# Kernel tuning notes

Measured on AMD Instinct MI355X. Metric: run time of the kernel, lower is better.

## Reference

```python
import jax, jax.numpy as jnp
import numpy as np

N_NODES = 50000
N_EDGES = 25000  # hyperedges
NNZ = 400000     # incidence pairs


def _segment_mean(x, idx, num_segments):
    s = jax.ops.segment_sum(x, idx, num_segments=num_segments)
    cnt = jax.ops.segment_sum(jnp.ones((x.shape[0], 1), x.dtype), idx, num_segments=num_segments)
    return s / jnp.maximum(cnt, 1.0)


def _unigcn_conv(X, W, vertex, edges, degE, degV):
    # X: [N, Cin] -> [N, Cout]
    X = X @ W                                   # linear (no bias)
    Xve = X[vertex]                             # gather per incidence [nnz, C]
    Xe = _segment_mean(Xve, edges, N_EDGES)     # first_aggregate='mean' over hyperedges
    Xe = Xe * degE                              # [M,1] scale
    Xev = Xe[edges]                             # gather back [nnz, C]
    Xv = jax.ops.segment_sum(Xev, vertex, num_segments=N_NODES)
    return Xv * degV                            # [N,1] scale


def setup_inputs() -> dict:
    key = jax.random.key(0)
    ks = jax.random.split(key, 8)
    nfeat, nhid_total, nclass = 512, 512, 40
    def glorot(k, fan_in, fan_out):
        std = np.sqrt(6.0 / (fan_in + fan_out))
        return jax.random.uniform(k, (fan_in, fan_out), jnp.float32, -std, std)
    return {
        "X": jax.random.normal(ks[0], (N_NODES, nfeat), jnp.float32),
        "vertex": jax.random.randint(ks[1], (NNZ,), 0, N_NODES, jnp.int32),
        "edges": jax.random.randint(ks[2], (NNZ,), 0, N_EDGES, jnp.int32),
        "W1": glorot(ks[3], nfeat, nhid_total),
        "W2": glorot(ks[4], nhid_total, nhid_total),
        "Wout": glorot(ks[5], nhid_total, nclass),
        "degE": jax.random.uniform(ks[6], (N_EDGES, 1), jnp.float32, 0.1, 1.0),
        "degV": jax.random.uniform(ks[7], (N_NODES, 1), jnp.float32, 0.1, 1.0),
    }


def reference(X, vertex, edges, W1, W2, Wout, degE, degV):
    # dropout layers are identity at eval (rates = 0)
    X = jax.nn.relu(_unigcn_conv(X, W1, vertex, edges, degE, degV))
    X = jax.nn.relu(_unigcn_conv(X, W2, vertex, edges, degE, degV))
    X = _unigcn_conv(X, Wout, vertex, edges, degE, degV)
    return jax.nn.log_softmax(X, axis=1)
```

## Files before the change

kernel.cpp:

```cpp
#include <hip/hip_runtime.h>

#define N_NODES 50000
#define N_EDGES_C 25000
#define NNZ_C 400000
#define SCHUNK 2048

typedef __bf16 bf16;
typedef __bf16 bf16x8 __attribute__((ext_vector_type(8)));
typedef __bf16 bf16x4 __attribute__((ext_vector_type(4)));
typedef float f32x4 __attribute__((ext_vector_type(4)));

typedef __attribute__((address_space(1))) const void as1_cvoid;
typedef __attribute__((address_space(3))) void as3_void;

__device__ __forceinline__ void gload_lds16(const bf16* g, bf16* l) {
  __builtin_amdgcn_global_load_lds((as1_cvoid*)g, (as3_void*)l, 16, 0, 0);
}

__global__ void hist_kernel(const int* __restrict__ vtx, const int* __restrict__ edg,
                            int* __restrict__ cntV, int* __restrict__ cntE, int nnz) {
  int i = blockIdx.x * blockDim.x + threadIdx.x;
  if (i < nnz) {
    atomicAdd(&cntV[vtx[i]], 1);
    atomicAdd(&cntE[edg[i]], 1);
  }
}

__global__ void scan_part2(const int* __restrict__ cntE, const int* __restrict__ cntV,
                           int* __restrict__ partE, int* __restrict__ partV,
                           int nbE) {
  __shared__ int red[256];
  const int t = threadIdx.x;
  const int isV = (blockIdx.x >= nbE);
  const int b = isV ? (blockIdx.x - nbE) : blockIdx.x;
  const int* cnt = isV ? cntV : cntE;
  const int n = isV ? N_NODES : N_EDGES_C;
  const int base = b * SCHUNK + t * 8;
  int s = 0;
#pragma unroll
  for (int q = 0; q < 8; ++q) {
    int i = base + q;
    if (i < n) s += cnt[i];
  }
  red[t] = s;
  __syncthreads();
  for (int d = 128; d > 0; d >>= 1) {
    if (t < d) red[t] += red[t + d];
    __syncthreads();
  }
  if (t == 0) (isV ? partV : partE)[b] = red[0];
}

__global__ void scan_mid2(int* __restrict__ partE, int* __restrict__ partV,
                          int* __restrict__ eoff, int* __restrict__ voff,
                          int nbE, int nbV) {
  const int wv = threadIdx.x >> 6;
  const int lane = threadIdx.x & 63;
  int* part = wv ? partV : partE;
  int* off = wv ? voff : eoff;
  const int np = wv ? nbV : nbE;
  const int n = wv ? N_NODES : N_EDGES_C;
  int orig = (lane < np) ? part[lane] : 0;
  int v = orig;
  for (int o = 1; o < 64; o <<= 1) {
    int x = __shfl_up(v, o);
    if (lane >= o) v += x;
  }
  if (lane < np) part[lane] = v - orig;
  if (lane == 63) off[n] = v;
}

__global__ void scan_final2(const int* __restrict__ cntE, const int* __restrict__ cntV,
                            const int* __restrict__ partE, const int* __restrict__ partV,
                            int* __restrict__ eoff, int* __restrict__ voff, int nbE) {
  __shared__ int tsum[256];
  const int t = threadIdx.x;
  const int isV = (blockIdx.x >= nbE);
  const int b = isV ? (blockIdx.x - nbE) : blockIdx.x;
  const int* cnt = isV ? cntV : cntE;
  const int* part = isV ? partV : partE;
  int* off = isV ? voff : eoff;
  const int n = isV ? N_NODES : N_EDGES_C;
  const int base = b * SCHUNK + t * 8;
  int loc[8];
  int s = 0;
#pragma unroll
  for (int q = 0; q < 8; ++q) {
    int i = base + q;
    loc[q] = (i < n) ? cnt[i] : 0;
    s += loc[q];
  }
  tsum[t] = s;
  __syncthreads();
  for (int d = 1; d < 256; d <<= 1) {
    int x = (t >= d) ? tsum[t - d] : 0;
    __syncthreads();
    tsum[t] += x;
    __syncthreads();
  }
  int run = part[b] + ((t > 0) ? tsum[t - 1] : 0);
#pragma unroll
  for (int q = 0; q < 8; ++q) {
    int i = base + q;
    if (i < n) off[i] = run;
    run += loc[q];
  }
}

__global__ void scatter_kernel(const int* __restrict__ vtx, const int* __restrict__ edg,
                               const int* __restrict__ eoff, const int* __restrict__ voff,
                               int* __restrict__ curE, int* __restrict__ curV,
                               int* __restrict__ evtx, int* __restrict__ vedg, int nnz) {
  int i = blockIdx.x * blockDim.x + threadIdx.x;
  if (i < nnz) {
    int e = edg[i], v = vtx[i];
    int p = atomicAdd(&curE[e], 1);
    evtx[eoff[e] + p] = v;
    int q = atomicAdd(&curV[v], 1);
    vedg[voff[v] + q] = e;
  }
}

__global__ void prep_conv(const float* __restrict__ W1, const float* __restrict__ W2,
                          const float* __restrict__ Wout, const float* __restrict__ X,
                          bf16* __restrict__ Wt1, bf16* __restrict__ Wt2,
                          bf16* __restrict__ Wt3, bf16* __restrict__ Xb) {
  const int b = blockIdx.x;
  const int t = threadIdx.x;
  if (b < 1024) {
    int idx = b * 256 + t;
    int n = idx >> 9, k = idx & 511;
    Wt1[idx] = (bf16)W1[(size_t)k * 512 + n];
  } else if (b < 2048) {
    int idx = (b - 1024) * 256 + t;
    int n = idx >> 9, k = idx & 511;
    Wt2[idx] = (bf16)W2[(size_t)k * 512 + n];
  } else if (b < 2304) {
    int idx = (b - 2048) * 256 + t;
    int n = idx >> 9, k = idx & 511;
    Wt3[idx] = (n < 40) ? (bf16)Wout[(size_t)k * 40 + n] : (bf16)0.0f;
  } else {
    size_t i = ((size_t)(b - 2304) * 256 + t) * 8;
    float4 v0 = *(const float4*)(X + i);
    float4 v1 = *(const float4*)(X + i + 4);
    bf16x8 o;
    o[0] = (bf16)v0.x; o[1] = (bf16)v0.y; o[2] = (bf16)v0.z; o[3] = (bf16)v0.w;
    o[4] = (bf16)v1.x; o[5] = (bf16)v1.y; o[6] = (bf16)v1.z; o[7] = (bf16)v1.w;
    *(bf16x8*)(Xb + i) = o;
  }
}

template <int BF16OUT>
__global__ __launch_bounds__(256) void gemm_bf16_kernel(
    const bf16* __restrict__ A, const bf16* __restrict__ B,
    float* __restrict__ Cf, bf16* __restrict__ Cb, int M, int K, int ldC, int Nstore) {
  __shared__ bf16 Al[2][128][64];
  __shared__ bf16 Bl[2][128][64];
  const int t = threadIdx.x;
  const int n0 = blockIdx.x * 128;
  const int m0 = blockIdx.y * 128;
  const int w = t >> 6, lane = t & 63;
  const int wr = w >> 1, wc = w & 1;
  const int lr = lane & 15;
  const int ls = lane >> 4;

  f32x4 acc[4][4];
#pragma unroll
  for (int m = 0; m < 4; ++m)
#pragma unroll
    for (int n = 0; n < 4; ++n) acc[m][n] = (f32x4){0.f, 0.f, 0.f, 0.f};

  const int srow8 = lane >> 3;
  const int scol = ((lane & 7) ^ srow8) << 3;

  const bf16* Abase = A + (size_t)m0 * K;
  const bf16* Bbase = B + (size_t)n0 * K;

#define STAGE(tile, bsel)                                                        \
  {                                                                              \
    const int kk_ = (tile) * 64;                                                 \
    _Pragma("unroll")                                                            \
    for (int q = 0; q < 4; ++q) {                                                \
      const int row = w * 32 + q * 8 + srow8;                                    \
      gload_lds16(Abase + (size_t)row * K + kk_ + scol, &Al[bsel][w*32+q*8][0]); \
      gload_lds16(Bbase + (size_t)row * K + kk_ + scol, &Bl[bsel][w*32+q*8][0]); \
    }                                                                            \
  }

  const int NT = K >> 6;
  STAGE(0, 0);
  for (int tt = 0; tt < NT; ++tt) {
    const int cur = tt & 1;
    if (tt + 1 < NT) {
      STAGE(tt + 1, cur ^ 1);
      asm volatile("s_waitcnt vmcnt(8)" ::: "memory");
    } else {
      asm volatile("s_waitcnt vmcnt(0)" ::: "memory");
    }
    __builtin_amdgcn_s_barrier();
    __builtin_amdgcn_s_setprio(1);
#pragma unroll
    for (int ks = 0; ks < 2; ++ks) {
      bf16x8 af[4], bfr[4];
#pragma unroll
      for (int m = 0; m < 4; ++m) {
        const int R = wr * 64 + m * 16 + lr;
        af[m] = *(const bf16x8*)(&Al[cur][R][((ks * 4 + ls) ^ (lr & 7)) << 3]);
      }
#pragma unroll
      for (int n = 0; n < 4; ++n) {
        const int R = wc * 64 + n * 16 + lr;
        bfr[n] = *(const bf16x8*)(&Bl[cur][R][((ks * 4 + ls) ^ (lr & 7)) << 3]);
      }
#pragma unroll
      for (int m = 0; m < 4; ++m)
#pragma unroll
        for (int n = 0; n < 4; ++n)
          acc[m][n] = __builtin_amdgcn_mfma_f32_16x16x32_bf16(af[m], bfr[n], acc[m][n], 0, 0, 0);
    }
    __builtin_amdgcn_s_setprio(0);
    __builtin_amdgcn_s_barrier();
  }
#undef STAGE

  const int cr = (lane >> 4) << 2;
  const int cc = lane & 15;
#pragma unroll
  for (int m = 0; m < 4; ++m) {
#pragma unroll
    for (int n = 0; n < 4; ++n) {
      int gc = n0 + wc * 64 + n * 16 + cc;
      if (gc >= Nstore) continue;
#pragma unroll
      for (int i = 0; i < 4; ++i) {
        int gr = m0 + wr * 64 + m * 16 + cr + i;
        if (gr < M) {
          if (BF16OUT) Cb[(size_t)gr * ldC + gc] = (bf16)acc[m][n][i];
          else         Cf[(size_t)gr * ldC + gc] = acc[m][n][i];
        }
      }
    }
  }
}

__global__ __launch_bounds__(256) void edge_agg_w(
    const bf16* __restrict__ Y, const int* __restrict__ eoff, const int* __restrict__ evtx,
    const float* __restrict__ degE, bf16* __restrict__ Xe, int nE) {
  const int wv = (blockIdx.x * 256 + threadIdx.x) >> 6;
  if (wv >= nE) return;
  const int lane = threadIdx.x & 63;
  const int beg = eoff[wv], end = eoff[wv + 1];
  const int cnt = end - beg;
  const float scale = (cnt > 0) ? degE[wv] / (float)cnt : 0.f;
  float acc[8] = {0.f, 0.f, 0.f, 0.f, 0.f, 0.f, 0.f, 0.f};
  for (int base = beg; base < end; base += 64) {
    const int nb = min(64, end - base);
    int myidx = (lane < nb) ? evtx[base + lane] : 0;
    int j = 0;
    for (; j + 1 < nb; j += 2) {
      const int i0 = __shfl(myidx, j);
      const int i1 = __shfl(myidx, j + 1);
      bf16x8 v0 = *(const bf16x8*)(Y + (size_t)i0 * 512 + lane * 8);
      bf16x8 v1 = *(const bf16x8*)(Y + (size_t)i1 * 512 + lane * 8);
#pragma unroll
      for (int q = 0; q < 8; ++q) acc[q] += (float)v0[q] + (float)v1[q];
    }
    if (j < nb) {
      const int i0 = __shfl(myidx, j);
      bf16x8 v0 = *(const bf16x8*)(Y + (size_t)i0 * 512 + lane * 8);
#pragma unroll
      for (int q = 0; q < 8; ++q) acc[q] += (float)v0[q];
    }
  }
  bf16x8 o;
#pragma unroll
  for (int q = 0; q < 8; ++q) o[q] = (bf16)(acc[q] * scale);
  *(bf16x8*)(Xe + (size_t)wv * 512 + lane * 8) = o;
}

__global__ __launch_bounds__(256) void vtx_agg_w(
    const bf16* __restrict__ Xe, const int* __restrict__ voff, const int* __restrict__ vedg,
    const float* __restrict__ degV, bf16* __restrict__ outB, int nV) {
  const int wv = (blockIdx.x * 256 + threadIdx.x) >> 6;
  if (wv >= nV) return;
  const int lane = threadIdx.x & 63;
  const int beg = voff[wv], end = voff[wv + 1];
  const float dv = degV[wv];
  float acc[8] = {0.f, 0.f, 0.f, 0.f, 0.f, 0.f, 0.f, 0.f};
  for (int base = beg; base < end; base += 64) {
    const int nb = min(64, end - base);
    int myidx = (lane < nb) ? vedg[base + lane] : 0;
    int j = 0;
    for (; j + 1 < nb; j += 2) {
      const int i0 = __shfl(myidx, j);
      const int i1 = __shfl(myidx, j + 1);
      bf16x8 v0 = *(const bf16x8*)(Xe + (size_t)i0 * 512 + lane * 8);
      bf16x8 v1 = *(const bf16x8*)(Xe + (size_t)i1 * 512 + lane * 8);
#pragma unroll
      for (int q = 0; q < 8; ++q) acc[q] += (float)v0[q] + (float)v1[q];
    }
    if (j < nb) {
      const int i0 = __shfl(myidx, j);
      bf16x8 v0 = *(const bf16x8*)(Xe + (size_t)i0 * 512 + lane * 8);
#pragma unroll
      for (int q = 0; q < 8; ++q) acc[q] += (float)v0[q];
    }
  }
  bf16x8 o;
#pragma unroll
  for (int q = 0; q < 8; ++q) o[q] = (bf16)fmaxf(acc[q] * dv, 0.f);
  *(bf16x8*)(outB + (size_t)wv * 512 + lane * 8) = o;
}

__global__ __launch_bounds__(256) void edge_agg40_w(
    const bf16* __restrict__ Y, const int* __restrict__ eoff, const int* __restrict__ evtx,
    const float* __restrict__ degE, bf16* __restrict__ Xe, int nE) {
  const int wv = (blockIdx.x * 256 + threadIdx.x) >> 6;
  if (wv >= nE) return;
  const int lane = threadIdx.x & 63;
  const int beg = eoff[wv], end = eoff[wv + 1];
  const int cnt = end - beg;
  const float scale = (cnt > 0) ? degE[wv] / (float)cnt : 0.f;
  float a0 = 0.f;
  for (int base = beg; base < end; base += 64) {
    const int nb = min(64, end - base);
    int myidx = (lane < nb) ? evtx[base + lane] : 0;
    int j = 0;
    for (; j + 3 < nb; j += 4) {
      const int i0 = __shfl(myidx, j);
      const int i1 = __shfl(myidx, j + 1);
      const int i2 = __shfl(myidx, j + 2);
      const int i3 = __shfl(myidx, j + 3);
      if (lane < 40) {
        float x0 = (float)Y[(size_t)i0 * 40 + lane];
        float x1 = (float)Y[(size_t)i1 * 40 + lane];
        float x2 = (float)Y[(size_t)i2 * 40 + lane];
        float x3 = (float)Y[(size_t)i3 * 40 + lane];
        a0 += (x0 + x1) + (x2 + x3);
      }
    }
    for (; j < nb; ++j) {
      const int i0 = __shfl(myidx, j);
      if (lane < 40) a0 += (float)Y[(size_t)i0 * 40 + lane];
    }
  }
  if (lane < 40) Xe[(size_t)wv * 40 + lane] = (bf16)(a0 * scale);
}

__global__ __launch_bounds__(256) void vtx_agg_lsm(
    const bf16* __restrict__ Xe, const int* __restrict__ voff, const int* __restrict__ vedg,
    const float* __restrict__ degV, float* __restrict__ out, int nV) {
  const int wv = (blockIdx.x * 256 + threadIdx.x) >> 6;
  if (wv >= nV) return;
  const int lane = threadIdx.x & 63;
  const int beg = voff[wv], end = voff[wv + 1];
  const float dv = degV[wv];
  float a0 = 0.f;
  for (int base = beg; base < end; base += 64) {
    const int nb = min(64, end - base);
    int myidx = (lane < nb) ? vedg[base + lane] : 0;
    int j = 0;
    for (; j + 3 < nb; j += 4) {
      const int i0 = __shfl(myidx, j);
      const int i1 = __shfl(myidx, j + 1);
      const int i2 = __shfl(myidx, j + 2);
      const int i3 = __shfl(myidx, j + 3);
      if (lane < 40) {
        float x0 = (float)Xe[(size_t)i0 * 40 + lane];
        float x1 = (float)Xe[(size_t)i1 * 40 + lane];
        float x2 = (float)Xe[(size_t)i2 * 40 + lane];
        float x3 = (float)Xe[(size_t)i3 * 40 + lane];
        a0 += (x0 + x1) + (x2 + x3);
      }
    }
    for (; j < nb; ++j) {
      const int i0 = __shfl(myidx, j);
      if (lane < 40) a0 += (float)Xe[(size_t)i0 * 40 + lane];
    }
  }
  a0 *= dv;
  float val = (lane < 40) ? a0 : -3.4e38f;
  float m = val;
#pragma unroll
  for (int o = 32; o > 0; o >>= 1) m = fmaxf(m, __shfl_xor(m, o));
  float ex = (lane < 40) ? expf(val - m) : 0.f;
  float s = ex;
#pragma unroll
  for (int o = 32; o > 0; o >>= 1) s += __shfl_xor(s, o);
  float ls = logf(s);
  if (lane < 40) out[(size_t)wv * 40 + lane] = val - m - ls;
}

extern "C" void kernel_launch(void* const* d_in, const int* in_sizes, int n_in,
                              void* d_out, int out_size, void* d_ws, size_t ws_size,
                              hipStream_t stream) {
  (void)in_sizes; (void)n_in; (void)out_size; (void)ws_size;
  const float* X = (const float*)d_in[0];
  const int* vertex = (const int*)d_in[1];
  const int* edges = (const int*)d_in[2];
  const float* W1 = (const float*)d_in[3];
  const float* W2 = (const float*)d_in[4];
  const float* Wout = (const float*)d_in[5];
  const float* degE = (const float*)d_in[6];
  const float* degV = (const float*)d_in[7];
  float* out = (float*)d_out;

  char* ws = (char*)d_ws;
  size_t off = 0;
  auto alloc = [&](size_t bytes) -> void* {
    void* p = ws + off;
    off += (bytes + 255) & ~(size_t)255;
    return p;
  };
  bf16* Xb  = (bf16*)alloc((size_t)N_NODES * 512 * sizeof(bf16));
  bf16* Yb  = (bf16*)alloc((size_t)N_NODES * 512 * sizeof(bf16));
  bf16* XeB = (bf16*)alloc((size_t)N_EDGES_C * 512 * sizeof(bf16));
  bf16* Y40b  = (bf16*)alloc((size_t)N_NODES * 40 * sizeof(bf16));
  bf16* Xe40b = (bf16*)alloc((size_t)N_EDGES_C * 40 * sizeof(bf16));
  bf16* Wt1 = (bf16*)alloc((size_t)512 * 512 * sizeof(bf16));
  bf16* Wt2 = (bf16*)alloc((size_t)512 * 512 * sizeof(bf16));
  bf16* Wt3 = (bf16*)alloc((size_t)128 * 512 * sizeof(bf16));
  int* eoff = (int*)alloc((N_EDGES_C + 1) * sizeof(int));
  int* voff = (int*)alloc((N_NODES + 1) * sizeof(int));
  int* evtx = (int*)alloc((size_t)NNZ_C * sizeof(int));
  int* vedg = (int*)alloc((size_t)NNZ_C * sizeof(int));
  int* cnts = (int*)alloc((size_t)(2 * (N_EDGES_C + N_NODES)) * sizeof(int));
  int* cntE = cnts;
  int* cntV = cnts + N_EDGES_C;
  int* curE = cnts + N_EDGES_C + N_NODES;
  int* curV = cnts + 2 * N_EDGES_C + N_NODES;
  int* partE = (int*)alloc(64 * sizeof(int));
  int* partV = (int*)alloc(64 * sizeof(int));

  hipMemsetAsync(cnts, 0, (size_t)(2 * (N_EDGES_C + N_NODES)) * sizeof(int), stream);

  prep_conv<<<2304 + 12500, 256, 0, stream>>>(W1, W2, Wout, X, Wt1, Wt2, Wt3, Xb);

  hist_kernel<<<(NNZ_C + 255) / 256, 256, 0, stream>>>(vertex, edges, cntV, cntE, NNZ_C);

  const int nbE = (N_EDGES_C + SCHUNK - 1) / SCHUNK;
  const int nbV = (N_NODES + SCHUNK - 1) / SCHUNK;
  scan_part2<<<nbE + nbV, 256, 0, stream>>>(cntE, cntV, partE, partV, nbE);
  scan_mid2<<<1, 128, 0, stream>>>(partE, partV, eoff, voff, nbE, nbV);
  scan_final2<<<nbE + nbV, 256, 0, stream>>>(cntE, cntV, partE, partV, eoff, voff, nbE);

  scatter_kernel<<<(NNZ_C + 255) / 256, 256, 0, stream>>>(vertex, edges, eoff, voff,
                                                          curE, curV, evtx, vedg, NNZ_C);

  const int MB = (N_NODES + 127) / 128;

  {
    dim3 g(4, MB);
    gemm_bf16_kernel<1><<<g, 256, 0, stream>>>(Xb, Wt1, nullptr, Yb, N_NODES, 512, 512, 512);
  }
  edge_agg_w<<<(N_EDGES_C + 3) / 4, 256, 0, stream>>>(Yb, eoff, evtx, degE, XeB, N_EDGES_C);
  vtx_agg_w<<<(N_NODES + 3) / 4, 256, 0, stream>>>(XeB, voff, vedg, degV, Xb, N_NODES);

  {
    dim3 g(4, MB);
    gemm_bf16_kernel<1><<<g, 256, 0, stream>>>(Xb, Wt2, nullptr, Yb, N_NODES, 512, 512, 512);
  }
  edge_agg_w<<<(N_EDGES_C + 3) / 4, 256, 0, stream>>>(Yb, eoff, evtx, degE, XeB, N_EDGES_C);
  vtx_agg_w<<<(N_NODES + 3) / 4, 256, 0, stream>>>(XeB, voff, vedg, degV, Xb, N_NODES);

  {
    dim3 g(1, MB);
    gemm_bf16_kernel<1><<<g, 256, 0, stream>>>(Xb, Wt3, nullptr, Y40b, N_NODES, 512, 40, 40);
  }
  edge_agg40_w<<<(N_EDGES_C + 3) / 4, 256, 0, stream>>>(Y40b, eoff, evtx, degE, Xe40b, N_EDGES_C);
  vtx_agg_lsm<<<(N_NODES + 3) / 4, 256, 0, stream>>>(Xe40b, voff, vedg, degV, out, N_NODES);
}
```

Before: 511.7 us.

## Add XCD-aware block swizzle and narrow-N GEMM tile for output layer

The GEMM now uses a 1D grid remapped so consecutive logical tiles land on the same XCD, which should improve L2 reuse of A rows across the four N tiles. The GEMM is templated on the N tile width, and the 40-column output layer uses a 64-wide B tile so it stops computing and loading a mostly-zero 128-wide tile. The float-output path is dropped. The padded grid adds some early-exit blocks.

```diff
diff --git a/kernel.cpp b/kernel.cpp
--- a/kernel.cpp
+++ b/kernel.cpp
@@ -150,23 +150,34 @@
   }
 }
 
-template <int BF16OUT>
+template <int TN>
 __global__ __launch_bounds__(256) void gemm_bf16_kernel(
     const bf16* __restrict__ A, const bf16* __restrict__ B,
-    float* __restrict__ Cf, bf16* __restrict__ Cb, int M, int K, int ldC, int Nstore) {
+    bf16* __restrict__ Cb, int M, int K, int ldC, int Nstore) {
   __shared__ bf16 Al[2][128][64];
-  __shared__ bf16 Bl[2][128][64];
+  __shared__ bf16 Bl[2][TN][64];
+  const int bid = blockIdx.x;
+  const int cpx = gridDim.x >> 3;
+  const int wid = (bid & 7) * cpx + (bid >> 3);
+  const int MBLK = (M + 127) >> 7;
+  int mIdx, nIdx;
+  if (TN == 128) { mIdx = wid >> 2; nIdx = wid & 3; }
+  else           { mIdx = wid;      nIdx = 0; }
+  if (mIdx >= MBLK) return;
+  const int m0 = mIdx * 128;
+  const int n0 = nIdx * TN;
+
   const int t = threadIdx.x;
-  const int n0 = blockIdx.x * 128;
-  const int m0 = blockIdx.y * 128;
   const int w = t >> 6, lane = t & 63;
-  const int wr = w >> 1, wc = w & 1;
+  const int rb = (TN == 128) ? ((w >> 1) * 64) : (w * 32);
+  const int cb = (TN == 128) ? ((w & 1) * 64) : 0;
+  const int MF = (TN == 128) ? 4 : 2;
   const int lr = lane & 15;
   const int ls = lane >> 4;
 
-  f32x4 acc[4][4];
-#pragma unroll
-  for (int m = 0; m < 4; ++m)
+  f32x4 acc[(TN == 128) ? 4 : 2][4];
+#pragma unroll
+  for (int m = 0; m < MF; ++m)
 #pragma unroll
     for (int n = 0; n < 4; ++n) acc[m][n] = (f32x4){0.f, 0.f, 0.f, 0.f};
 
@@ -176,15 +187,20 @@
   const bf16* Abase = A + (size_t)m0 * K;
   const bf16* Bbase = B + (size_t)n0 * K;
 
-#define STAGE(tile, bsel)                                                        \
-  {                                                                              \
-    const int kk_ = (tile) * 64;                                                 \
-    _Pragma("unroll")                                                            \
-    for (int q = 0; q < 4; ++q) {                                                \
-      const int row = w * 32 + q * 8 + srow8;                                    \
-      gload_lds16(Abase + (size_t)row * K + kk_ + scol, &Al[bsel][w*32+q*8][0]); \
-      gload_lds16(Bbase + (size_t)row * K + kk_ + scol, &Bl[bsel][w*32+q*8][0]); \
-    }                                                                            \
+#define STAGE(tile, bsel)                                                          \
+  {                                                                                \
+    const int kk_ = (tile) * 64;                                                   \
+    _Pragma("unroll")                                                              \
+    for (int q = 0; q < 4; ++q) {                                                  \
+      const int row = w * 32 + q * 8 + srow8;                                      \
+      gload_lds16(Abase + (size_t)row * K + kk_ + scol, &Al[bsel][w*32+q*8][0]);   \
+    }                                                                              \
+    _Pragma("unroll")                                                              \
+    for (int q = 0; q < TN / 32; ++q) {                                            \
+      const int row = w * (TN / 4) + q * 8 + srow8;                                \
+      gload_lds16(Bbase + (size_t)row * K + kk_ + scol,                            \
+                  &Bl[bsel][w * (TN / 4) + q * 8][0]);                             \
+    }                                                                              \
   }
 
   const int NT = K >> 6;
@@ -193,7 +209,8 @@
     const int cur = tt & 1;
     if (tt + 1 < NT) {
       STAGE(tt + 1, cur ^ 1);
-      asm volatile("s_waitcnt vmcnt(8)" ::: "memory");
+      if (TN == 128) asm volatile("s_waitcnt vmcnt(8)" ::: "memory");
+      else           asm volatile("s_waitcnt vmcnt(6)" ::: "memory");
     } else {
       asm volatile("s_waitcnt vmcnt(0)" ::: "memory");
     }
@@ -201,19 +218,19 @@
     __builtin_amdgcn_s_setprio(1);
 #pragma unroll
     for (int ks = 0; ks < 2; ++ks) {
-      bf16x8 af[4], bfr[4];
-#pragma unroll
-      for (int m = 0; m < 4; ++m) {
-        const int R = wr * 64 + m * 16 + lr;
+      bf16x8 af[(TN == 128) ? 4 : 2], bfr[4];
+#pragma unroll
+      for (int m = 0; m < MF; ++m) {
+        const int R = rb + m * 16 + lr;
         af[m] = *(const bf16x8*)(&Al[cur][R][((ks * 4 + ls) ^ (lr & 7)) << 3]);
       }
 #pragma unroll
       for (int n = 0; n < 4; ++n) {
-        const int R = wc * 64 + n * 16 + lr;
+        const int R = cb + n * 16 + lr;
         bfr[n] = *(const bf16x8*)(&Bl[cur][R][((ks * 4 + ls) ^ (lr & 7)) << 3]);
       }
 #pragma unroll
-      for (int m = 0; m < 4; ++m)
+      for (int m = 0; m < MF; ++m)
 #pragma unroll
         for (int n = 0; n < 4; ++n)
           acc[m][n] = __builtin_amdgcn_mfma_f32_16x16x32_bf16(af[m], bfr[n], acc[m][n], 0, 0, 0);
@@ -226,18 +243,15 @@
   const int cr = (lane >> 4) << 2;
   const int cc = lane & 15;
 #pragma unroll
-  for (int m = 0; m < 4; ++m) {
+  for (int m = 0; m < MF; ++m) {
 #pragma unroll
     for (int n = 0; n < 4; ++n) {
-      int gc = n0 + wc * 64 + n * 16 + cc;
+      int gc = n0 + cb + n * 16 + cc;
       if (gc >= Nstore) continue;
 #pragma unroll
       for (int i = 0; i < 4; ++i) {
-        int gr = m0 + wr * 64 + m * 16 + cr + i;
-        if (gr < M) {
-          if (BF16OUT) Cb[(size_t)gr * ldC + gc] = (bf16)acc[m][n][i];
-          else         Cf[(size_t)gr * ldC + gc] = acc[m][n][i];
-        }
+        int gr = m0 + rb + m * 16 + cr + i;
+        if (gr < M) Cb[(size_t)gr * ldC + gc] = (bf16)acc[m][n][i];
       }
     }
   }
@@ -448,25 +462,18 @@
                                                           curE, curV, evtx, vedg, NNZ_C);
 
   const int MB = (N_NODES + 127) / 128;
-
-  {
-    dim3 g(4, MB);
-    gemm_bf16_kernel<1><<<g, 256, 0, stream>>>(Xb, Wt1, nullptr, Yb, N_NODES, 512, 512, 512);
-  }
+  const int G512 = ((MB * 4 + 7) / 8) * 8;
+  const int G64  = ((MB + 7) / 8) * 8;
+
+  gemm_bf16_kernel<128><<<G512, 256, 0, stream>>>(Xb, Wt1, Yb, N_NODES, 512, 512, 512);
   edge_agg_w<<<(N_EDGES_C + 3) / 4, 256, 0, stream>>>(Yb, eoff, evtx, degE, XeB, N_EDGES_C);
   vtx_agg_w<<<(N_NODES + 3) / 4, 256, 0, stream>>>(XeB, voff, vedg, degV, Xb, N_NODES);
 
-  {
-    dim3 g(4, MB);
-    gemm_bf16_kernel<1><<<g, 256, 0, stream>>>(Xb, Wt2, nullptr, Yb, N_NODES, 512, 512, 512);
-  }
+  gemm_bf16_kernel<128><<<G512, 256, 0, stream>>>(Xb, Wt2, Yb, N_NODES, 512, 512, 512);
   edge_agg_w<<<(N_EDGES_C + 3) / 4, 256, 0, stream>>>(Yb, eoff, evtx, degE, XeB, N_EDGES_C);
   vtx_agg_w<<<(N_NODES + 3) / 4, 256, 0, stream>>>(XeB, voff, vedg, degV, Xb, N_NODES);
 
-  {
-    dim3 g(1, MB);
-    gemm_bf16_kernel<1><<<g, 256, 0, stream>>>(Xb, Wt3, nullptr, Y40b, N_NODES, 512, 40, 40);
-  }
+  gemm_bf16_kernel<64><<<G64, 256, 0, stream>>>(Xb, Wt3, Y40b, N_NODES, 512, 40, 40);
   edge_agg40_w<<<(N_EDGES_C + 3) / 4, 256, 0, stream>>>(Y40b, eoff, evtx, degE, Xe40b, N_EDGES_C);
   vtx_agg_lsm<<<(N_NODES + 3) / 4, 256, 0, stream>>>(Xe40b, voff, vedg, degV, out, N_NODES);
 }
```

New measurement: 498.8 us. 1.03x faster.
